# Kernel tuning notes

Measured on AMD Instinct MI355X. Metric: run time of the kernel, lower is better.

Reference implementation:

```python
import jax, jax.numpy as jnp
import numpy as np

B, N, FV_IN, FV_OUT, FE_IN, FE_OUT = 32, 128, 128, 128, 128, 128


def setup_inputs() -> dict:
    key = jax.random.key(0)
    ks = jax.random.split(key, 8)
    s = lambda fan_in: 1.0 / np.sqrt(fan_in)
    return {
        "v_in": jax.random.normal(ks[0], (B, N, FV_IN), dtype=jnp.float32),
        "e_in": jax.random.normal(ks[1], (B, N, N, FE_IN), dtype=jnp.float32),
        # e_vert_layer: Linear(vert_f_in, edge_f_out)
        "W_ev": jax.random.uniform(ks[2], (FV_IN, FE_OUT), jnp.float32, -s(FV_IN), s(FV_IN)),
        "b_ev": jax.random.uniform(ks[3], (FE_OUT,), jnp.float32, -s(FV_IN), s(FV_IN)),
        # e_layer: Linear(edge_f_in, edge_f_out)
        "W_e": jax.random.uniform(ks[4], (FE_IN, FE_OUT), jnp.float32, -s(FE_IN), s(FE_IN)),
        "b_e": jax.random.uniform(ks[5], (FE_OUT,), jnp.float32, -s(FE_IN), s(FE_IN)),
        # v_layer: Linear(vert_f_in + edge_f_out, vert_f_out)
        "W_v": jax.random.uniform(ks[6], (FV_IN + FE_OUT, FV_OUT), jnp.float32, -s(FV_IN + FE_OUT), s(FV_IN + FE_OUT)),
        "b_v": jax.random.uniform(ks[7], (FV_OUT,), jnp.float32, -s(FV_IN + FE_OUT), s(FV_IN + FE_OUT)),
    }


def reference(v_in, e_in, W_ev, b_ev, W_e, b_e, W_v, b_v):
    # per-vertex projection to edge feature space: [B, N, FE_OUT]
    e_v = jnp.einsum("bnf,fg->bng", v_in, W_ev) + b_ev
    # outer vertex sum broadcast: [B, N, N, FE_OUT]
    outer_v_sum = e_v[:, None, :, :] + e_v[:, :, None, :]
    # edge projection: [B, N, N, FE_OUT]
    e = jnp.einsum("bmnf,fg->bmng", e_in, W_e) + b_e
    e_out = jax.nn.relu(e + outer_v_sum)
    # sum-aggregate over dim 1 -> per-vertex edge summary [B, N, FE_OUT]
    per_v_e = jnp.sum(e_out, axis=1)
    vert_e_combined = jnp.concatenate([per_v_e, v_in], axis=2)
    v = jnp.einsum("bnf,fg->bng", vert_e_combined, W_v) + b_v
    v_out = jax.nn.relu(v)
    return (v_out, e_out)
```

## Files before the change

### kernel.cpp

```cpp
#include <hip/hip_runtime.h>
#include <cstdint>
#include <cstring>

#define B_ 32
#define N_ 128
#define F_ 128

typedef __attribute__((ext_vector_type(8))) __bf16 bf16x8;
typedef __attribute__((ext_vector_type(4))) float f32x4;

__device__ inline uint16_t f2bf_bits(float f) {
  __bf16 h = (__bf16)f;
  uint16_t u;
  __builtin_memcpy(&u, &h, 2);
  return u;
}

__global__ __launch_bounds__(128) void ev_kernel(const float* __restrict__ v_in,
                                                 const float* __restrict__ W_ev,
                                                 const float* __restrict__ b_ev,
                                                 float* __restrict__ e_v) {
  __shared__ float vr[8][F_];
  const int R0 = blockIdx.x * 8;
  const int tid = threadIdx.x;
#pragma unroll
  for (int i = 0; i < 8; ++i) vr[i][tid] = v_in[(size_t)(R0 + i) * F_ + tid];
  __syncthreads();
  float acc[8];
  const float bb = b_ev[tid];
#pragma unroll
  for (int i = 0; i < 8; ++i) acc[i] = bb;
  for (int f = 0; f < F_; ++f) {
    const float wv = W_ev[f * F_ + tid];
#pragma unroll
    for (int i = 0; i < 8; ++i) acc[i] += vr[i][f] * wv;
  }
#pragma unroll
  for (int i = 0; i < 8; ++i) e_v[(size_t)(R0 + i) * F_ + tid] = acc[i];
}

__global__ void pack_kernel(const float* __restrict__ W_e, uint32_t* __restrict__ wp) {
  const int tid = threadIdx.x;
  for (int idx = tid; idx < 2048; idx += 256) {
    const int t = idx >> 6, l = idx & 63;
    const int kt = t >> 3, gt = t & 7;
    const int kbase = kt * 32 + ((l >> 4) << 3);
    const int g = gt * 16 + (l & 15);
#pragma unroll
    for (int p = 0; p < 4; ++p) {
      const uint32_t lo = f2bf_bits(W_e[(kbase + 2 * p) * F_ + g]);
      const uint32_t hi = f2bf_bits(W_e[(kbase + 2 * p + 1) * F_ + g]);
      wp[idx * 4 + p] = lo | (hi << 16);
    }
  }
}

__global__ __launch_bounds__(512) void main_kernel(
    const float* __restrict__ v_in, const float* __restrict__ e_in,
    const float* __restrict__ e_v, const float* __restrict__ b_e,
    const float* __restrict__ W_v, const float* __restrict__ b_v,
    const bf16x8* __restrict__ wp, float* __restrict__ v_out,
    float* __restrict__ e_out) {
  __shared__ bf16x8 wfrag[2048];
  __shared__ float comb[16][256];

  const int tid = threadIdx.x;
  const int w = tid >> 6, l = tid & 63;
  const int b = blockIdx.x >> 3;
  const int n0 = (blockIdx.x & 7) * 16;
  const int lr = (l >> 4) << 2;
  const int lc = l & 15;

  for (int i = tid; i < 2048; i += 512) wfrag[i] = wp[i];

  float evr[8][4];
  const float* evb = e_v + (size_t)(b * N_ + n0) * F_;
#pragma unroll
  for (int gt = 0; gt < 8; ++gt) {
    const int g = gt * 16 + lc;
    const float be = b_e[g];
#pragma unroll
    for (int q = 0; q < 4; ++q) evr[gt][q] = evb[(size_t)(lr + q) * F_ + g] + be;
  }

  float pve[8][4];
#pragma unroll
  for (int gt = 0; gt < 8; ++gt)
#pragma unroll
    for (int q = 0; q < 4; ++q) pve[gt][q] = 0.f;

  __syncthreads();

  const float* einb = e_in + (size_t)b * N_ * N_ * F_;
  float* eoutb = e_out + (size_t)b * N_ * N_ * F_;
  const float* evmb = e_v + (size_t)b * N_ * F_ + lc;

  for (int it = 0; it < 16; ++it) {
    const int m = w + (it << 3);
    const float* rowp = einb + (size_t)(m * N_ + n0 + lc) * F_ + ((l >> 4) << 3);
    f32x4 fa0[4], fa1[4];
#pragma unroll
    for (int kt = 0; kt < 4; ++kt) {
      fa0[kt] = *reinterpret_cast<const f32x4*>(rowp + kt * 32);
      fa1[kt] = *reinterpret_cast<const f32x4*>(rowp + kt * 32 + 4);
    }
    float evm[8];
#pragma unroll
    for (int gt = 0; gt < 8; ++gt) evm[gt] = evmb[(size_t)m * F_ + gt * 16];

    bf16x8 a[4];
#pragma unroll
    for (int kt = 0; kt < 4; ++kt) {
#pragma unroll
      for (int e = 0; e < 4; ++e) {
        a[kt][e] = (__bf16)fa0[kt][e];
        a[kt][e + 4] = (__bf16)fa1[kt][e];
      }
    }

    f32x4 acc[8];
#pragma unroll
    for (int gt = 0; gt < 8; ++gt) {
      acc[gt][0] = 0.f; acc[gt][1] = 0.f; acc[gt][2] = 0.f; acc[gt][3] = 0.f;
    }
#pragma unroll
    for (int kt = 0; kt < 4; ++kt)
#pragma unroll
      for (int gt = 0; gt < 8; ++gt)
        acc[gt] = __builtin_amdgcn_mfma_f32_16x16x32_bf16(
            a[kt], wfrag[(kt * 8 + gt) * 64 + l], acc[gt], 0, 0, 0);

    float* outp = eoutb + (size_t)(m * N_ + n0) * F_;
#pragma unroll
    for (int gt = 0; gt < 8; ++gt) {
      const int g = gt * 16 + lc;
#pragma unroll
      for (int q = 0; q < 4; ++q) {
        float v = acc[gt][q] + evr[gt][q] + evm[gt];
        v = fmaxf(v, 0.f);
        pve[gt][q] += v;
        outp[(size_t)(lr + q) * F_ + g] = v;
      }
    }
  }

  for (int t = 0; t < 8; ++t) {
    if (w == t) {
#pragma unroll
      for (int gt = 0; gt < 8; ++gt) {
        const int g = gt * 16 + lc;
#pragma unroll
        for (int q = 0; q < 4; ++q) {
          if (t == 0) comb[lr + q][g] = pve[gt][q];
          else comb[lr + q][g] += pve[gt][q];
        }
      }
    }
    __syncthreads();
  }

  for (int idx = tid; idx < 2048; idx += 512) {
    const int r = idx >> 7, f = idx & 127;
    comb[r][128 + f] = v_in[(size_t)(b * N_ + n0 + r) * F_ + f];
  }
  __syncthreads();

  const int g = tid & 127, qr = tid >> 7;
  float a0, a1, a2, a3;
  const float bvv = b_v[g];
  a0 = a1 = a2 = a3 = bvv;
  for (int f = 0; f < 256; ++f) {
    const float wv = W_v[f * F_ + g];
    a0 += comb[qr * 4 + 0][f] * wv;
    a1 += comb[qr * 4 + 1][f] * wv;
    a2 += comb[qr * 4 + 2][f] * wv;
    a3 += comb[qr * 4 + 3][f] * wv;
  }
  float* vo = v_out + (size_t)(b * N_ + n0 + qr * 4) * F_ + g;
  vo[0 * F_] = fmaxf(a0, 0.f);
  vo[1 * F_] = fmaxf(a1, 0.f);
  vo[2 * F_] = fmaxf(a2, 0.f);
  vo[3 * F_] = fmaxf(a3, 0.f);
}

extern "C" void kernel_launch(void* const* d_in, const int* in_sizes, int n_in,
                              void* d_out, int out_size, void* d_ws, size_t ws_size,
                              hipStream_t stream) {
  const float* v_in = (const float*)d_in[0];
  const float* e_in = (const float*)d_in[1];
  const float* W_ev = (const float*)d_in[2];
  const float* b_ev = (const float*)d_in[3];
  const float* W_e  = (const float*)d_in[4];
  const float* b_e  = (const float*)d_in[5];
  const float* W_v  = (const float*)d_in[6];
  const float* b_v  = (const float*)d_in[7];

  float* out = (float*)d_out;
  float* v_out = out;
  float* e_out = out + (size_t)B_ * N_ * F_;

  float* e_v = (float*)d_ws;
  uint32_t* wpack = (uint32_t*)((char*)d_ws + (size_t)B_ * N_ * F_ * 4);

  ev_kernel<<<(B_ * N_) / 8, 128, 0, stream>>>(v_in, W_ev, b_ev, e_v);
  pack_kernel<<<1, 256, 0, stream>>>(W_e, wpack);
  main_kernel<<<B_ * 8, 512, 0, stream>>>(v_in, e_in, e_v, b_e, W_v, b_v,
                                          (const bf16x8*)wpack, v_out, e_out);
}
```

Before: 179.1 us.

## Split edge kernel across m-chunks, transpose MFMA output, move vertex GEMM to separate kernel

Main kernel now runs with 4x more blocks of 256 threads: each block handles a quarter of the m rows and writes per-split partial column sums to a workspace buffer. A new v_kernel reduces those partials and does the vertex linear layer. The MFMA operands are swapped so each lane holds 4 consecutive features, which allows float4 stores of e_out and float4 loads of e_v. The weight pack also now runs on 8 blocks. The intent is higher occupancy and memory-level parallelism on the bandwidth-bound edge pass (1024 blocks instead of 256) and wider stores. The cost is an extra kernel launch and a partial-sum round trip through global memory.

```diff
diff --git a/kernel.cpp b/kernel.cpp
--- a/kernel.cpp
+++ b/kernel.cpp
@@ -5,6 +5,7 @@
 #define B_ 32
 #define N_ 128
 #define F_ 128
+#define SPLIT_ 4
 
 typedef __attribute__((ext_vector_type(8))) __bf16 bf16x8;
 typedef __attribute__((ext_vector_type(4))) float f32x4;
@@ -40,74 +41,64 @@
 }
 
 __global__ void pack_kernel(const float* __restrict__ W_e, uint32_t* __restrict__ wp) {
-  const int tid = threadIdx.x;
-  for (int idx = tid; idx < 2048; idx += 256) {
-    const int t = idx >> 6, l = idx & 63;
-    const int kt = t >> 3, gt = t & 7;
-    const int kbase = kt * 32 + ((l >> 4) << 3);
-    const int g = gt * 16 + (l & 15);
-#pragma unroll
-    for (int p = 0; p < 4; ++p) {
-      const uint32_t lo = f2bf_bits(W_e[(kbase + 2 * p) * F_ + g]);
-      const uint32_t hi = f2bf_bits(W_e[(kbase + 2 * p + 1) * F_ + g]);
-      wp[idx * 4 + p] = lo | (hi << 16);
-    }
-  }
-}
-
-__global__ __launch_bounds__(512) void main_kernel(
-    const float* __restrict__ v_in, const float* __restrict__ e_in,
-    const float* __restrict__ e_v, const float* __restrict__ b_e,
-    const float* __restrict__ W_v, const float* __restrict__ b_v,
-    const bf16x8* __restrict__ wp, float* __restrict__ v_out,
-    float* __restrict__ e_out) {
+  const int idx = blockIdx.x * 256 + threadIdx.x;
+  const int t = idx >> 6, l = idx & 63;
+  const int kt = t >> 3, gt = t & 7;
+  const int kbase = kt * 32 + ((l >> 4) << 3);
+  const int g = gt * 16 + (l & 15);
+#pragma unroll
+  for (int p = 0; p < 4; ++p) {
+    const uint32_t lo = f2bf_bits(W_e[(kbase + 2 * p) * F_ + g]);
+    const uint32_t hi = f2bf_bits(W_e[(kbase + 2 * p + 1) * F_ + g]);
+    wp[idx * 4 + p] = lo | (hi << 16);
+  }
+}
+
+__global__ __launch_bounds__(256, 4) void main_kernel(
+    const float* __restrict__ e_in, const float* __restrict__ e_v,
+    const float* __restrict__ b_e, const bf16x8* __restrict__ wp,
+    float* __restrict__ e_out, float* __restrict__ pve_part) {
   __shared__ bf16x8 wfrag[2048];
-  __shared__ float comb[16][256];
+  __shared__ float comb[16][132];
 
   const int tid = threadIdx.x;
   const int w = tid >> 6, l = tid & 63;
-  const int b = blockIdx.x >> 3;
-  const int n0 = (blockIdx.x & 7) * 16;
+  const int bid = blockIdx.x;
+  const int s = bid & 3;
+  const int nt = (bid >> 2) & 7;
+  const int b = bid >> 5;
+  const int n0 = nt * 16;
   const int lr = (l >> 4) << 2;
   const int lc = l & 15;
 
-  for (int i = tid; i < 2048; i += 512) wfrag[i] = wp[i];
-
-  float evr[8][4];
-  const float* evb = e_v + (size_t)(b * N_ + n0) * F_;
+  for (int i = tid; i < 2048; i += 256) wfrag[i] = wp[i];
+
+  for (int i = tid; i < 2048; i += 256) {
+    const int r = i >> 7, g = i & 127;
+    comb[r][g] = e_v[((size_t)(b * N_ + n0) + r) * F_ + g] + b_e[g];
+  }
+
+  f32x4 pve[8];
 #pragma unroll
   for (int gt = 0; gt < 8; ++gt) {
-    const int g = gt * 16 + lc;
-    const float be = b_e[g];
-#pragma unroll
-    for (int q = 0; q < 4; ++q) evr[gt][q] = evb[(size_t)(lr + q) * F_ + g] + be;
-  }
-
-  float pve[8][4];
-#pragma unroll
-  for (int gt = 0; gt < 8; ++gt)
-#pragma unroll
-    for (int q = 0; q < 4; ++q) pve[gt][q] = 0.f;
+    pve[gt][0] = 0.f; pve[gt][1] = 0.f; pve[gt][2] = 0.f; pve[gt][3] = 0.f;
+  }
 
   __syncthreads();
 
   const float* einb = e_in + (size_t)b * N_ * N_ * F_;
   float* eoutb = e_out + (size_t)b * N_ * N_ * F_;
-  const float* evmb = e_v + (size_t)b * N_ * F_ + lc;
-
-  for (int it = 0; it < 16; ++it) {
-    const int m = w + (it << 3);
-    const float* rowp = einb + (size_t)(m * N_ + n0 + lc) * F_ + ((l >> 4) << 3);
+  const float* evmb = e_v + (size_t)b * N_ * F_;
+
+  for (int it = 0; it < 8; ++it) {
+    const int m = s * 32 + it * 4 + w;
+    const float* rowp = einb + ((size_t)m * N_ + n0 + lc) * F_ + ((l >> 4) << 3);
     f32x4 fa0[4], fa1[4];
 #pragma unroll
     for (int kt = 0; kt < 4; ++kt) {
       fa0[kt] = *reinterpret_cast<const f32x4*>(rowp + kt * 32);
       fa1[kt] = *reinterpret_cast<const f32x4*>(rowp + kt * 32 + 4);
     }
-    float evm[8];
-#pragma unroll
-    for (int gt = 0; gt < 8; ++gt) evm[gt] = evmb[(size_t)m * F_ + gt * 16];
-
     bf16x8 a[4];
 #pragma unroll
     for (int kt = 0; kt < 4; ++kt) {
@@ -128,59 +119,72 @@
 #pragma unroll
       for (int gt = 0; gt < 8; ++gt)
         acc[gt] = __builtin_amdgcn_mfma_f32_16x16x32_bf16(
-            a[kt], wfrag[(kt * 8 + gt) * 64 + l], acc[gt], 0, 0, 0);
-
-    float* outp = eoutb + (size_t)(m * N_ + n0) * F_;
+            wfrag[(kt * 8 + gt) * 64 + l], a[kt], acc[gt], 0, 0, 0);
+
+    const float* evmr = evmb + (size_t)m * F_;
+    float* outp = eoutb + ((size_t)m * N_ + n0 + lc) * F_;
 #pragma unroll
     for (int gt = 0; gt < 8; ++gt) {
-      const int g = gt * 16 + lc;
-#pragma unroll
-      for (int q = 0; q < 4; ++q) {
-        float v = acc[gt][q] + evr[gt][q] + evm[gt];
-        v = fmaxf(v, 0.f);
-        pve[gt][q] += v;
-        outp[(size_t)(lr + q) * F_ + g] = v;
+      const f32x4 evm = *reinterpret_cast<const f32x4*>(evmr + gt * 16 + lr);
+      const f32x4 evn = *reinterpret_cast<const f32x4*>(&comb[lc][gt * 16 + lr]);
+      f32x4 v = acc[gt] + evn + evm;
+#pragma unroll
+      for (int q = 0; q < 4; ++q) v[q] = fmaxf(v[q], 0.f);
+      pve[gt] += v;
+      *reinterpret_cast<f32x4*>(outp + gt * 16 + lr) = v;
+    }
+  }
+
+  __syncthreads();
+  for (int t = 0; t < 4; ++t) {
+    if (w == t) {
+#pragma unroll
+      for (int gt = 0; gt < 8; ++gt) {
+        f32x4* cp = reinterpret_cast<f32x4*>(&comb[lc][gt * 16 + lr]);
+        if (t == 0) *cp = pve[gt];
+        else *cp += pve[gt];
       }
     }
-  }
-
-  for (int t = 0; t < 8; ++t) {
-    if (w == t) {
-#pragma unroll
-      for (int gt = 0; gt < 8; ++gt) {
-        const int g = gt * 16 + lc;
-#pragma unroll
-        for (int q = 0; q < 4; ++q) {
-          if (t == 0) comb[lr + q][g] = pve[gt][q];
-          else comb[lr + q][g] += pve[gt][q];
-        }
-      }
-    }
     __syncthreads();
   }
 
-  for (int idx = tid; idx < 2048; idx += 512) {
-    const int r = idx >> 7, f = idx & 127;
-    comb[r][128 + f] = v_in[(size_t)(b * N_ + n0 + r) * F_ + f];
-  }
-  __syncthreads();
-
-  const int g = tid & 127, qr = tid >> 7;
-  float a0, a1, a2, a3;
-  const float bvv = b_v[g];
-  a0 = a1 = a2 = a3 = bvv;
+  float* pp = pve_part + (((size_t)s * B_ + b) * N_ + n0) * F_;
+  for (int i = tid; i < 512; i += 256) {
+    const int r = i >> 5, c = (i & 31) << 2;
+    reinterpret_cast<f32x4*>(pp)[i] = *reinterpret_cast<f32x4*>(&comb[r][c]);
+  }
+}
+
+__global__ __launch_bounds__(128) void v_kernel(
+    const float* __restrict__ v_in, const float* __restrict__ pve_part,
+    const float* __restrict__ W_v, const float* __restrict__ b_v,
+    float* __restrict__ v_out) {
+  __shared__ float rows[8][256];
+  const int R0 = blockIdx.x * 8;
+  const int tid = threadIdx.x;
+#pragma unroll
+  for (int i = 0; i < 8; ++i) {
+    const size_t r = R0 + i;
+    float acc = 0.f;
+#pragma unroll
+    for (int s = 0; s < SPLIT_; ++s)
+      acc += pve_part[((size_t)s * B_ * N_ + r) * F_ + tid];
+    rows[i][tid] = acc;
+    rows[i][128 + tid] = v_in[r * F_ + tid];
+  }
+  __syncthreads();
+  float acc[8];
+  const float bb = b_v[tid];
+#pragma unroll
+  for (int i = 0; i < 8; ++i) acc[i] = bb;
   for (int f = 0; f < 256; ++f) {
-    const float wv = W_v[f * F_ + g];
-    a0 += comb[qr * 4 + 0][f] * wv;
-    a1 += comb[qr * 4 + 1][f] * wv;
-    a2 += comb[qr * 4 + 2][f] * wv;
-    a3 += comb[qr * 4 + 3][f] * wv;
-  }
-  float* vo = v_out + (size_t)(b * N_ + n0 + qr * 4) * F_ + g;
-  vo[0 * F_] = fmaxf(a0, 0.f);
-  vo[1 * F_] = fmaxf(a1, 0.f);
-  vo[2 * F_] = fmaxf(a2, 0.f);
-  vo[3 * F_] = fmaxf(a3, 0.f);
+    const float wv = W_v[f * F_ + tid];
+#pragma unroll
+    for (int i = 0; i < 8; ++i) acc[i] += rows[i][f] * wv;
+  }
+#pragma unroll
+  for (int i = 0; i < 8; ++i)
+    v_out[(size_t)(R0 + i) * F_ + tid] = fmaxf(acc[i], 0.f);
 }
 
 extern "C" void kernel_launch(void* const* d_in, const int* in_sizes, int n_in,
@@ -199,11 +203,15 @@
   float* v_out = out;
   float* e_out = out + (size_t)B_ * N_ * F_;
 
-  float* e_v = (float*)d_ws;
-  uint32_t* wpack = (uint32_t*)((char*)d_ws + (size_t)B_ * N_ * F_ * 4);
+  char* ws = (char*)d_ws;
+  float* e_v = (float*)ws;
+  uint32_t* wpack = (uint32_t*)(ws + (size_t)2097152);
+  float* pve_part = (float*)(ws + (size_t)2097152 + 65536);
 
   ev_kernel<<<(B_ * N_) / 8, 128, 0, stream>>>(v_in, W_ev, b_ev, e_v);
-  pack_kernel<<<1, 256, 0, stream>>>(W_e, wpack);
-  main_kernel<<<B_ * 8, 512, 0, stream>>>(v_in, e_in, e_v, b_e, W_v, b_v,
-                                          (const bf16x8*)wpack, v_out, e_out);
-}
+  pack_kernel<<<8, 256, 0, stream>>>(W_e, wpack);
+  main_kernel<<<B_ * 8 * SPLIT_, 256, 0, stream>>>(e_in, e_v, b_e,
+                                                   (const bf16x8*)wpack,
+                                                   e_out, pve_part);
+  v_kernel<<<(B_ * N_) / 8, 128, 0, stream>>>(v_in, pve_part, W_v, b_v, v_out);
+}
```

Measured after the change: 191.6 us. 7.0% more time.
